# Optimization experiments

Hardware: AMD Instinct MI355X
Metric: run time of the kernel (lower is better)

## Reference

```python
import jax, jax.numpy as jnp
import numpy as np

V, D, C, NUM_CLASSES = 50000, 128, 128, 200
N, S = 4096, 128
NUM_VIDEOS = 256
KSIZES = (3, 4, 5)


def setup_inputs() -> dict:
    key = jax.random.key(0)
    ks = jax.random.split(key, 10)
    input_x = jax.random.randint(ks[0], (N, 1, S), 0, V)
    # sorted segment ids, every video non-empty (contiguous ragged segments)
    segment_ids = ((jnp.arange(N) * NUM_VIDEOS) // N).astype(jnp.int32)
    emb = jax.random.normal(ks[1], (V, D), dtype=jnp.float32) * (2.0 / (V + D)) ** 0.5  # xavier_normal
    W3 = jax.random.normal(ks[2], (3, D, C), dtype=jnp.float32) * 0.05
    b3 = jnp.zeros((C,), dtype=jnp.float32)
    W4 = jax.random.normal(ks[3], (4, D, C), dtype=jnp.float32) * 0.05
    b4 = jnp.zeros((C,), dtype=jnp.float32)
    W5 = jax.random.normal(ks[4], (5, D, C), dtype=jnp.float32) * 0.05
    b5 = jnp.zeros((C,), dtype=jnp.float32)
    Wout = jax.random.normal(ks[5], (3 * C, NUM_CLASSES), dtype=jnp.float32) * 0.05
    bout = jnp.zeros((NUM_CLASSES,), dtype=jnp.float32)
    return {"input_x": input_x, "segment_ids": segment_ids, "emb": emb,
            "W3": W3, "b3": b3, "W4": W4, "b4": b4, "W5": W5, "b5": b5,
            "Wout": Wout, "bout": bout}


def _conv_maxpool(x, W, b):
    # x: [N, S, D], W: [w, D, C] -> conv over time (VALID), then max over time -> [N, C]
    y = jax.lax.conv_general_dilated(x, W, window_strides=(1,), padding='VALID',
                                     dimension_numbers=('NWC', 'WIO', 'NWC')) + b
    return jnp.max(y, axis=1)


def reference(input_x, segment_ids, emb, W3, b3, W4, b4, W5, b5, Wout, bout):
    x = emb[input_x[:, 0, :]]                       # [N, S, D]
    feat = jnp.concatenate([_conv_maxpool(x, W3, b3),
                            _conv_maxpool(x, W4, b4),
                            _conv_maxpool(x, W5, b5)], axis=1)  # [N, 3C]
    logits = feat @ Wout + bout                     # [N, num_classes]
    scores = jax.nn.sigmoid(logits)
    # ragged per-video max over contiguous text rows
    video_scores = jax.ops.segment_max(scores, segment_ids, num_segments=NUM_VIDEOS)
    return video_scores
```

## Files before the change

kernel.cpp:

```cpp
#include <hip/hip_runtime.h>
#include <hip/hip_bf16.h>


using bf16_t   = __bf16;
using bf16x4   = __attribute__((ext_vector_type(4))) __bf16;
using bf16x8   = __attribute__((ext_vector_type(8))) __bf16;
using floatx4  = __attribute__((ext_vector_type(4))) float;
using floatx16 = __attribute__((ext_vector_type(16))) float;

#define N_SENT 4096
#define S_LEN  128
#define D_DIM  128
#define C_DIM  128
#define NCLS   200
#define NVID   256
#define V_SZ   50000

#define X_ROWS   132
#define X_STRIDE 136

#define BP3_OFF 0
#define BP4_OFF 49152
#define BP5_OFF 114688
#define BPACK_ELEMS 196608
#define EMB_BLOCKS   6250
#define BPACK_BLOCKS 768

#define FEAT_OFF  (1u << 20)
#define EMB16_OFF (8u << 20)

__global__ void prep(const float* __restrict__ emb, bf16_t* __restrict__ emb16,
                     const float* __restrict__ W3, const float* __restrict__ W4,
                     const float* __restrict__ W5, bf16_t* __restrict__ bpack) {
  const int b = blockIdx.x;
  if (b < EMB_BLOCKS) {
    const int i4 = b * 256 + threadIdx.x;
    const floatx4 f = __builtin_nontemporal_load((const floatx4*)emb + i4);
    bf16x4 h;
    h.x = (bf16_t)f.x; h.y = (bf16_t)f.y; h.z = (bf16_t)f.z; h.w = (bf16_t)f.w;
    __builtin_nontemporal_store(h, (bf16x4*)emb16 + i4);
    return;
  }
  const int idx = (b - EMB_BLOCKS) * 256 + threadIdx.x;
  if (idx >= BPACK_ELEMS) return;
  int KS; const float* W; int rel;
  if (idx < BP4_OFF)      { KS = 3; W = W3; rel = idx; }
  else if (idx < BP5_OFF) { KS = 4; W = W4; rel = idx - BP4_OFF; }
  else                    { KS = 5; W = W5; rel = idx - BP5_OFF; }
  int szct = 4096 * KS;
  int ct   = rel / szct;
  int r2   = rel - ct * szct;
  int sg   = r2 >> 9;
  int r3   = r2 & 511;
  int l    = r3 >> 3;
  int j    = r3 & 7;
  int kk   = sg * 16 + (l >> 5) * 8 + j;
  int c    = ct * 32 + (l & 31);
  bpack[idx] = (bf16_t)W[kk * C_DIM + c];
}

template <int KS>
__device__ __forceinline__ void conv32(const bf16_t* Abase,
                                       const bf16_t* bp,
                                       float* __restrict__ pmrow,
                                       int lane, int wm) {
  constexpr int BCT = 4096 * KS;
  floatx16 acc[2][2];
#pragma unroll
  for (int ct = 0; ct < 2; ++ct)
#pragma unroll
    for (int mt = 0; mt < 2; ++mt)
#pragma unroll
      for (int r = 0; r < 16; ++r) acc[ct][mt][r] = 0.f;

  const bf16_t* Ar = Abase;
#pragma unroll 1
  for (int c0 = 0; c0 < KS; ++c0) {
#pragma unroll
    for (int hf = 0; hf < 2; ++hf) {
      bf16x8 B0[4], B1[4];
#pragma unroll
      for (int s = 0; s < 4; ++s) {
        B0[s] = *(const bf16x8*)(bp + (hf * 4 + s) * 512);
        B1[s] = *(const bf16x8*)(bp + BCT + (hf * 4 + s) * 512);
      }
#pragma unroll
      for (int s = 0; s < 4; ++s) {
#pragma unroll
        for (int mt = 0; mt < 2; ++mt) {
          const bf16x8 a =
              *(const bf16x8*)(Ar + mt * 32 * X_STRIDE + (hf * 4 + s) * 16);
          acc[0][mt] = __builtin_amdgcn_mfma_f32_32x32x16_bf16(a, B0[s], acc[0][mt], 0, 0, 0);
          acc[1][mt] = __builtin_amdgcn_mfma_f32_32x32x16_bf16(a, B1[s], acc[1][mt], 0, 0, 0);
        }
      }
    }
    bp += 4096;
    Ar += X_STRIDE;
  }

  const int h = lane >> 5;
#pragma unroll
  for (int ct = 0; ct < 2; ++ct) {
    float mx = -__builtin_inff();
#pragma unroll
    for (int mt = 0; mt < 2; ++mt)
#pragma unroll
      for (int r = 0; r < 16; ++r) {
        const int row = (r & 3) + 8 * (r >> 2) + 4 * h;
        const bool valid = (wm == 0) | (mt == 0) | (96 + row < 129 - KS);
        if (valid) mx = fmaxf(mx, acc[ct][mt][r]);
      }
    mx = fmaxf(mx, __shfl_xor(mx, 32));
    if (lane < 32) pmrow[ct * 32 + lane] = mx;
  }
}

__global__ __launch_bounds__(256, 3) void conv_gemm(
    const int* __restrict__ input_x, const bf16_t* __restrict__ emb16,
    const bf16_t* __restrict__ bpack, const float* __restrict__ b3,
    const float* __restrict__ b4, const float* __restrict__ b5,
    float* __restrict__ feat) {
  __shared__ __align__(16) bf16_t Xs[X_ROWS * X_STRIDE];
  __shared__ float pm[3 * 2 * 128];
  const int sent = blockIdx.x;
  const int tid  = threadIdx.x;

  {
    const int rip = tid >> 4;
    const int l16 = tid & 15;
#pragma unroll
    for (int r0 = 0; r0 < S_LEN; r0 += 16) {
      const int row   = r0 + rip;
      const int token = __builtin_nontemporal_load(&input_x[sent * S_LEN + row]);
      const bf16x8 v  =
          __builtin_nontemporal_load((const bf16x8*)(emb16 + token * D_DIM + l16 * 8));
      *(bf16x8*)(&Xs[row * X_STRIDE + l16 * 8]) = v;
    }
    for (int i = tid; i < 4 * X_STRIDE; i += 256)
      Xs[128 * X_STRIDE + i] = (bf16_t)0.f;
  }
  __syncthreads();

  const int wv   = tid >> 6;
  const int lane = tid & 63;
  const int wm   = wv & 1;
  const int wc   = wv >> 1;

  const bf16_t* Abase =
      Xs + (wm * 64 + (lane & 31)) * X_STRIDE + (lane >> 5) * 8;
  const int blane = lane * 8;

  conv32<3>(Abase, bpack + BP3_OFF + 2 * wc * (4096 * 3) + blane,
            pm + (0 * 2 + wm) * 128 + wc * 64, lane, wm);
  __builtin_amdgcn_sched_barrier(0);
  conv32<4>(Abase, bpack + BP4_OFF + 2 * wc * (4096 * 4) + blane,
            pm + (1 * 2 + wm) * 128 + wc * 64, lane, wm);
  __builtin_amdgcn_sched_barrier(0);
  conv32<5>(Abase, bpack + BP5_OFF + 2 * wc * (4096 * 5) + blane,
            pm + (2 * 2 + wm) * 128 + wc * 64, lane, wm);
  __syncthreads();

  for (int i = tid; i < 384; i += 256) {
    const int kidx = i >> 7, c = i & 127;
    const float v = fmaxf(pm[(kidx * 2 + 0) * 128 + c],
                          pm[(kidx * 2 + 1) * 128 + c]);
    const float* bk = (kidx == 0) ? b3 : (kidx == 1) ? b4 : b5;
    __builtin_nontemporal_store(v + bk[c], &feat[sent * 384 + i]);
  }
}

__global__ void classify(const float* __restrict__ feat,
                         const float* __restrict__ Wout,
                         const float* __restrict__ bout,
                         float* __restrict__ out) {
  __shared__ float fs[16 * 384];
  const int vid = blockIdx.x;
  const int tid = threadIdx.x;
  for (int i = tid; i < 16 * 384; i += 256) fs[i] = feat[vid * 16 * 384 + i];
  __syncthreads();
  if (tid < NCLS) {
    float acc[16];
#pragma unroll
    for (int s = 0; s < 16; ++s) acc[s] = 0.f;
    for (int d = 0; d < 384; ++d) {
      const float wv = Wout[d * NCLS + tid];
#pragma unroll
      for (int s = 0; s < 16; ++s) acc[s] = fmaf(fs[s * 384 + d], wv, acc[s]);
    }
    const float b = bout[tid];
    float vmax = -__builtin_inff();
#pragma unroll
    for (int s = 0; s < 16; ++s) {
      const float sc = 1.f / (1.f + __expf(-(acc[s] + b)));
      vmax = fmaxf(vmax, sc);
    }
    out[vid * NCLS + tid] = vmax;
  }
}

extern "C" void kernel_launch(void* const* d_in, const int* in_sizes, int n_in,
                              void* d_out, int out_size, void* d_ws, size_t ws_size,
                              hipStream_t stream) {
  const int*   input_x = (const int*)d_in[0];
  const float* emb  = (const float*)d_in[2];
  const float* W3   = (const float*)d_in[3];
  const float* b3   = (const float*)d_in[4];
  const float* W4   = (const float*)d_in[5];
  const float* b4   = (const float*)d_in[6];
  const float* W5   = (const float*)d_in[7];
  const float* b5   = (const float*)d_in[8];
  const float* Wout = (const float*)d_in[9];
  const float* bout = (const float*)d_in[10];

  bf16_t* bpack = (bf16_t*)d_ws;
  float*  feat  = (float*)((char*)d_ws + FEAT_OFF);
  bf16_t* emb16 = (bf16_t*)((char*)d_ws + EMB16_OFF);
  float*  out   = (float*)d_out;

  prep<<<EMB_BLOCKS + BPACK_BLOCKS, 256, 0, stream>>>(emb, emb16, W3, W4, W5, bpack);
  conv_gemm<<<N_SENT, 256, 0, stream>>>(input_x, emb16, bpack, b3, b4, b5, feat);
  classify<<<NVID, 256, 0, stream>>>(feat, Wout, bout, out);
}
```

Before: 318.5 us.

## Use two waves per sentence covering all 128 rows, dropping shared-memory max reduction

The conv block shrinks from four waves to two. Each wave now computes all four 32-row M tiles for its 64 output channels, so every B fragment loaded from global memory is reused across twice as many MFMAs. Because no other wave shares its output, the shared-memory partial-max buffer and the final __syncthreads are gone, and each wave adds the bias and writes feat directly. The costs are twice as many accumulators per wave (more VGPR/AGPR pressure, launch bounds now 128 threads with 2 blocks per SM) and fewer waves to hide latency.

After: 314.5 us. Within noise of the previous version (-1.3%).

```diff
diff --git a/kernel.cpp b/kernel.cpp
--- a/kernel.cpp
+++ b/kernel.cpp
@@ -62,41 +62,39 @@
 template <int KS>
 __device__ __forceinline__ void conv32(const bf16_t* Abase,
                                        const bf16_t* bp,
-                                       float* __restrict__ pmrow,
-                                       int lane, int wm) {
-  constexpr int BCT = 4096 * KS;
-  floatx16 acc[2][2];
+                                       const float* __restrict__ bk,
+                                       float* __restrict__ frow,
+                                       int lane, int wc) {
+  constexpr int BCT    = 4096 * KS;
+  constexpr int NGROUP = 2 * KS;
+  floatx16 acc[2][4];
 #pragma unroll
   for (int ct = 0; ct < 2; ++ct)
 #pragma unroll
-    for (int mt = 0; mt < 2; ++mt)
+    for (int mt = 0; mt < 4; ++mt)
 #pragma unroll
       for (int r = 0; r < 16; ++r) acc[ct][mt][r] = 0.f;
 
   const bf16_t* Ar = Abase;
 #pragma unroll 1
-  for (int c0 = 0; c0 < KS; ++c0) {
-#pragma unroll
-    for (int hf = 0; hf < 2; ++hf) {
-      bf16x8 B0[4], B1[4];
-#pragma unroll
-      for (int s = 0; s < 4; ++s) {
-        B0[s] = *(const bf16x8*)(bp + (hf * 4 + s) * 512);
-        B1[s] = *(const bf16x8*)(bp + BCT + (hf * 4 + s) * 512);
+  for (int g = 0; g < NGROUP; ++g) {
+    bf16x8 B0[4], B1[4];
+#pragma unroll
+    for (int s = 0; s < 4; ++s) {
+      B0[s] = *(const bf16x8*)(bp + s * 512);
+      B1[s] = *(const bf16x8*)(bp + BCT + s * 512);
+    }
+#pragma unroll
+    for (int s = 0; s < 4; ++s) {
+#pragma unroll
+      for (int mt = 0; mt < 4; ++mt) {
+        const bf16x8 a = *(const bf16x8*)(Ar + mt * 32 * X_STRIDE + s * 16);
+        acc[0][mt] = __builtin_amdgcn_mfma_f32_32x32x16_bf16(a, B0[s], acc[0][mt], 0, 0, 0);
+        acc[1][mt] = __builtin_amdgcn_mfma_f32_32x32x16_bf16(a, B1[s], acc[1][mt], 0, 0, 0);
       }
-#pragma unroll
-      for (int s = 0; s < 4; ++s) {
-#pragma unroll
-        for (int mt = 0; mt < 2; ++mt) {
-          const bf16x8 a =
-              *(const bf16x8*)(Ar + mt * 32 * X_STRIDE + (hf * 4 + s) * 16);
-          acc[0][mt] = __builtin_amdgcn_mfma_f32_32x32x16_bf16(a, B0[s], acc[0][mt], 0, 0, 0);
-          acc[1][mt] = __builtin_amdgcn_mfma_f32_32x32x16_bf16(a, B1[s], acc[1][mt], 0, 0, 0);
-        }
-      }
-    }
-    bp += 4096;
-    Ar += X_STRIDE;
+    }
+    bp += 2048;
+    Ar += (g & 1) ? (X_STRIDE - 64) : 64;
   }
 
   const int h = lane >> 5;
@@ -104,25 +102,26 @@
   for (int ct = 0; ct < 2; ++ct) {
     float mx = -__builtin_inff();
 #pragma unroll
-    for (int mt = 0; mt < 2; ++mt)
+    for (int mt = 0; mt < 4; ++mt)
 #pragma unroll
       for (int r = 0; r < 16; ++r) {
         const int row = (r & 3) + 8 * (r >> 2) + 4 * h;
-        const bool valid = (wm == 0) | (mt == 0) | (96 + row < 129 - KS);
+        const bool valid = (mt < 3) | (row < 33 - KS);
         if (valid) mx = fmaxf(mx, acc[ct][mt][r]);
       }
     mx = fmaxf(mx, __shfl_xor(mx, 32));
-    if (lane < 32) pmrow[ct * 32 + lane] = mx;
-  }
-}
-
-__global__ __launch_bounds__(256, 3) void conv_gemm(
+    const int c = (2 * wc + ct) * 32 + (lane & 31);
+    if (lane < 32)
+      __builtin_nontemporal_store(mx + bk[c], &frow[c]);
+  }
+}
+
+__global__ __launch_bounds__(128, 2) void conv_gemm(
     const int* __restrict__ input_x, const bf16_t* __restrict__ emb16,
     const bf16_t* __restrict__ bpack, const float* __restrict__ b3,
     const float* __restrict__ b4, const float* __restrict__ b5,
     float* __restrict__ feat) {
   __shared__ __align__(16) bf16_t Xs[X_ROWS * X_STRIDE];
-  __shared__ float pm[3 * 2 * 128];
   const int sent = blockIdx.x;
   const int tid  = threadIdx.x;
 
@@ -130,44 +129,33 @@
     const int rip = tid >> 4;
     const int l16 = tid & 15;
 #pragma unroll
-    for (int r0 = 0; r0 < S_LEN; r0 += 16) {
+    for (int r0 = 0; r0 < S_LEN; r0 += 8) {
       const int row   = r0 + rip;
       const int token = __builtin_nontemporal_load(&input_x[sent * S_LEN + row]);
       const bf16x8 v  =
           __builtin_nontemporal_load((const bf16x8*)(emb16 + token * D_DIM + l16 * 8));
       *(bf16x8*)(&Xs[row * X_STRIDE + l16 * 8]) = v;
     }
-    for (int i = tid; i < 4 * X_STRIDE; i += 256)
+    for (int i = tid; i < 4 * X_STRIDE; i += 128)
       Xs[128 * X_STRIDE + i] = (bf16_t)0.f;
   }
   __syncthreads();
 
-  const int wv   = tid >> 6;
+  const int wc   = tid >> 6;
   const int lane = tid & 63;
-  const int wm   = wv & 1;
-  const int wc   = wv >> 1;
-
-  const bf16_t* Abase =
-      Xs + (wm * 64 + (lane & 31)) * X_STRIDE + (lane >> 5) * 8;
+
+  const bf16_t* Abase = Xs + (lane & 31) * X_STRIDE + (lane >> 5) * 8;
   const int blane = lane * 8;
-
-  conv32<3>(Abase, bpack + BP3_OFF + 2 * wc * (4096 * 3) + blane,
-            pm + (0 * 2 + wm) * 128 + wc * 64, lane, wm);
+  float* frow = feat + sent * 384;
+
+  conv32<3>(Abase, bpack + BP3_OFF + 2 * wc * (4096 * 3) + blane, b3,
+            frow, lane, wc);
   __builtin_amdgcn_sched_barrier(0);
-  conv32<4>(Abase, bpack + BP4_OFF + 2 * wc * (4096 * 4) + blane,
-            pm + (1 * 2 + wm) * 128 + wc * 64, lane, wm);
+  conv32<4>(Abase, bpack + BP4_OFF + 2 * wc * (4096 * 4) + blane, b4,
+            frow + 128, lane, wc);
   __builtin_amdgcn_sched_barrier(0);
-  conv32<5>(Abase, bpack + BP5_OFF + 2 * wc * (4096 * 5) + blane,
-            pm + (2 * 2 + wm) * 128 + wc * 64, lane, wm);
-  __syncthreads();
-
-  for (int i = tid; i < 384; i += 256) {
-    const int kidx = i >> 7, c = i & 127;
-    const float v = fmaxf(pm[(kidx * 2 + 0) * 128 + c],
-                          pm[(kidx * 2 + 1) * 128 + c]);
-    const float* bk = (kidx == 0) ? b3 : (kidx == 1) ? b4 : b5;
-    __builtin_nontemporal_store(v + bk[c], &feat[sent * 384 + i]);
-  }
+  conv32<5>(Abase, bpack + BP5_OFF + 2 * wc * (4096 * 5) + blane, b5,
+            frow + 256, lane, wc);
 }
 
 __global__ void classify(const float* __restrict__ feat,
@@ -219,6 +207,6 @@
   float*  out   = (float*)d_out;
 
   prep<<<EMB_BLOCKS + BPACK_BLOCKS, 256, 0, stream>>>(emb, emb16, W3, W4, W5, bpack);
-  conv_gemm<<<N_SENT, 256, 0, stream>>>(input_x, emb16, bpack, b3, b4, b5, feat);
+  conv_gemm<<<N_SENT, 128, 0, stream>>>(input_x, emb16, bpack, b3, b4, b5, feat);
   classify<<<NVID, 256, 0, stream>>>(feat, Wout, bout, out);
 }
```
